# Kernel tuning notes

Hardware: AMD Instinct MI355X
Metric: run time of the kernel (lower is better)

The kernel has to match this reference:

```python
import jax, jax.numpy as jnp
import numpy as np

SR = 22050
FL = 1024      # window_samples
FP = 256       # step_samples
FCEIL = 10000  # formant ceiling (Hz)
MAXF = 4       # max formants
AP_ORDER = 10
R_ORDER = 30
FMIN, FMAX = 50, 500
DK_ITERS = 60  # Durand-Kerner iterations (replaces companion-matrix eig; differentiable)

_w = np.blackman(FL)
WIN = jnp.asarray(_w / np.sqrt(np.sum(_w ** 2)), jnp.float32)  # power-normalized blackman (diffsptk default)


def _frame(x):
    # center-padded framing, frames = T//FP + 1
    pad = FL // 2
    xp = jnp.pad(x, ((0, 0), (pad, pad)))
    n_frames = x.shape[-1] // FP + 1
    idx = jnp.arange(n_frames)[:, None] * FP + jnp.arange(FL)[None, :]
    return xp[:, idx]  # [B, F, FL]


def _levinson(r, order):
    # Levinson-Durbin on autocorrelation r[..., :order+1].
    # Returns (allpole poly coeffs a[..., order+1] with a0=1, reflection coeffs k[..., order]).
    a = jnp.zeros(r.shape[:-1] + (order + 1,), r.dtype).at[..., 0].set(1.0)
    E = r[..., 0]
    ks = []
    for m in range(1, order + 1):
        if m == 1:
            acc = r[..., 1]
        else:
            acc = r[..., m] + jnp.sum(a[..., 1:m] * r[..., m - 1:0:-1], axis=-1)
        k = -acc / (E + 1e-9)
        a_prev = a
        a = a.at[..., m].set(k)
        if m > 1:
            a = a.at[..., 1:m].add(k[..., None] * a_prev[..., m - 1:0:-1])
        E = E * (1.0 - k * k)
        ks.append(k)
    return a, jnp.stack(ks, axis=-1)


def _poly_roots(coeffs):
    # Durand-Kerner simultaneous root iteration, vectorized over frames.
    n = coeffs.shape[-1] - 1
    c = (coeffs / coeffs[..., :1]).astype(jnp.complex64)
    z0 = (0.4 + 0.9j) ** jnp.arange(1, n + 1)
    z = jnp.broadcast_to(z0, c.shape[:-1] + (n,)).astype(jnp.complex64)
    eye = jnp.eye(n, dtype=jnp.complex64)
    def step(z, _):
        p = jnp.zeros_like(z)
        for i in range(n + 1):  # Horner eval of poly at all current root estimates
            p = p * z + c[..., i:i + 1]
        diff = z[..., :, None] - z[..., None, :] + eye
        z = z - p / (jnp.prod(diff, axis=-1) + 1e-12)
        return z, None
    z, _ = jax.lax.scan(step, z, None, length=DK_ITERS)
    return z  # [..., n]


def _root_to_formant(roots):
    # downsampled spectrum covers 0..FCEIL/2, so freq = angle/(2*pi)*FCEIL
    ang = jnp.angle(roots)
    freq = ang / (2.0 * jnp.pi) * FCEIL
    freq = jnp.where(ang > 1e-4, freq, FCEIL * 0.5)  # keep upper-half-plane roots only
    return jnp.sort(freq, axis=-1)[..., :MAXF]  # [B, F, MAXF]


def _pitch(x):
    # autocorrelation pitch tracker
    xf = _frame(x)
    spec = jnp.fft.rfft(xf)
    ac = jnp.fft.irfft(spec * jnp.conj(spec))
    lag_min, lag_max = SR // FMAX, SR // FMIN  # 44..441
    seg = ac[..., lag_min:lag_max + 1]
    peak = jnp.max(seg, axis=-1)
    idx = jnp.argmax(seg, axis=-1)
    nccf = peak / (ac[..., 0] + 1e-9)
    pitch = SR / (lag_min + idx).astype(jnp.float32)
    voicing = (nccf > 0.3).astype(jnp.float32)
    return pitch, voicing, nccf


def _forward(x):
    xf = _frame(x)                 # [B, F, FL]
    xw = xf * WIN
    spec = jnp.fft.rfft(xw)        # [B, F, 513]
    nb = spec.shape[-1]
    ds = int(FCEIL / SR * nb)      # 232 bins -> Nyquist FCEIL/2
    x_ds = spec[..., :ds]
    ac_ds = jnp.fft.irfft(x_ds * jnp.conj(x_ds))   # [B, F, 462]
    ac_us = jnp.fft.irfft(spec * jnp.conj(spec))   # [B, F, 1024]
    ap_env, _ = _levinson(ac_ds, AP_ORDER)
    _, r_coeff_ref = _levinson(ac_us, R_ORDER)
    roots = _poly_roots(ap_env)
    formants = _root_to_formant(roots)
    energy = 10.0 * jnp.log10(jnp.sum(xf * xf, axis=-1) + 1e-10)
    mag = jnp.abs(jnp.fft.rfft(xf))
    freqs = jnp.arange(nb, dtype=jnp.float32) * (SR / FL)
    centroid = jnp.sum(mag * freqs, axis=-1) / (jnp.sum(mag, axis=-1) + 1e-10)
    tilt = ac_ds[..., 1] / (ac_ds[..., 0] + 1e-10)
    pitch, voicing, nccf = _pitch(x)
    pitch = jnp.log(pitch)
    return (formants, energy, centroid, tilt, pitch, voicing, r_coeff_ref, x_ds, nccf)


def setup_inputs() -> dict:
    key = jax.random.key(0)
    x = jax.random.normal(key, (8, 661500), jnp.float32)
    return {"x": x}


def reference(x):
    return _forward(x)
```

## Files before the change

### kernel.cpp

```cpp
#include <hip/hip_runtime.h>
#include <math.h>

#define NSAMP   661500
#define NFRAME  2584
#define NFTOT   20672
#define FPB     6
#define NBLK    3446

#define EN_OFF    82688
#define CEN_OFF   103360
#define TILT_OFF  124032
#define PITCH_OFF 144704
#define VOI_OFF   165376
#define RC_OFF    186048
#define XDS_OFF   806208

__device__ __forceinline__ float waveReduceSum(float v) {
  #pragma unroll
  for (int m = 1; m < 64; m <<= 1) v += __shfl_xor(v, m, 64);
  return v;
}

__device__ __forceinline__ float blockReduceSum(float v, float* s) {
  v = waveReduceSum(v);
  const int w = threadIdx.x >> 6;
  if ((threadIdx.x & 63) == 0) s[w] = v;
  __syncthreads();
  v = s[0] + s[1] + s[2] + s[3];
  __syncthreads();
  return v;
}

__device__ __forceinline__ void blockReduceSum2(float& v0, float& v1, float* s) {
  v0 = waveReduceSum(v0);
  v1 = waveReduceSum(v1);
  const int w = threadIdx.x >> 6;
  if ((threadIdx.x & 63) == 0) { s[w] = v0; s[4 + w] = v1; }
  __syncthreads();
  v0 = s[0] + s[1] + s[2] + s[3];
  v1 = s[4] + s[5] + s[6] + s[7];
  __syncthreads();
}

__device__ __forceinline__ void fft1024p(float2* X, float2* Y, const float2* tw, int tid) {
  int m = 1;
  #pragma unroll
  for (int s = 0; s < 5; ++s) {
    const int k  = tid & (m - 1);
    const int jm = tid - k;
    const float2 a0 = X[tid];
    const float2 a1 = X[tid + 256];
    const float2 a2 = X[tid + 512];
    const float2 a3 = X[tid + 768];
    const float2 w1 = tw[jm];
    float2 sA, dA, sB, dB;
    sA.x = a0.x + a2.x; sA.y = a0.y + a2.y;
    { const float dx = a0.x - a2.x, dy = a0.y - a2.y;
      dA.x = dx * w1.x + dy * w1.y;
      dA.y = dy * w1.x - dx * w1.y; }
    sB.x = a1.x + a3.x; sB.y = a1.y + a3.y;
    { const float dx = a1.x - a3.x, dy = a1.y - a3.y;
      const float wx = -w1.y, wy = w1.x;
      dB.x = dx * wx + dy * wy;
      dB.y = dy * wx - dx * wy; }
    const float w2x = w1.x * w1.x - w1.y * w1.y;
    const float w2y = 2.0f * w1.x * w1.y;
    const int B = 4 * tid - 3 * k;
    { float2 o;
      o.x = sA.x + sB.x; o.y = sA.y + sB.y;
      Y[B] = o;
      const float dx = sA.x - sB.x, dy = sA.y - sB.y;
      o.x = dx * w2x + dy * w2y;
      o.y = dy * w2x - dx * w2y;
      Y[B + 2 * m] = o; }
    { float2 o;
      o.x = dA.x + dB.x; o.y = dA.y + dB.y;
      Y[B + m] = o;
      const float dx = dA.x - dB.x, dy = dA.y - dB.y;
      o.x = dx * w2x + dy * w2y;
      o.y = dy * w2x - dx * w2y;
      Y[B + 3 * m] = o; }
    __syncthreads();
    float2* tmp = X; X = Y; Y = tmp;
    m <<= 2;
  }
}

template<int ORDER>
__device__ __forceinline__ void levinson_d(const double* r, double* a) {
  double E = r[0];
  a[0] = 1.0;
  #pragma unroll
  for (int m = 1; m <= ORDER; ++m) {
    double acc = r[m];
    #pragma unroll
    for (int i = 1; i < m; ++i) acc += a[i] * r[m - i];
    const double kk = -acc / (E + 1e-9);
    #pragma unroll
    for (int i = 1; i <= (m - 1) / 2; ++i) {
      const double t1 = a[i], t2 = a[m - i];
      a[i]     = t1 + kk * t2;
      a[m - i] = t2 + kk * t1;
    }
    if ((m & 1) == 0) { const double t = a[m >> 1]; a[m >> 1] = t + kk * t; }
    a[m] = kk;
    E *= (1.0 - kk * kk);
  }
}

__device__ __forceinline__ void levinson_f30(const float* r, float* gk) {
  float a[31];
  float E = r[0];
  a[0] = 1.0f;
  #pragma unroll
  for (int m = 1; m <= 30; ++m) {
    float acc = r[m];
    #pragma unroll
    for (int i = 1; i < m; ++i) acc += a[i] * r[m - i];
    const float kk = -acc / (E + 1e-9f);
    #pragma unroll
    for (int i = 1; i <= (m - 1) / 2; ++i) {
      const float t1 = a[i], t2 = a[m - i];
      a[i]     = t1 + kk * t2;
      a[m - i] = t2 + kk * t1;
    }
    if ((m & 1) == 0) { const float t = a[m >> 1]; a[m >> 1] = t + kk * t; }
    a[m] = kk;
    E *= (1.0f - kk * kk);
    if (gk) gk[m - 1] = kk;
  }
}

__global__ void __launch_bounds__(256, 7)
feat_mono6(const float* __restrict__ x, float* __restrict__ out,
           const int xds_pf, const int nccf_off) {
  __shared__ float2 A[1024];
  __shared__ float2 Bb[1024];
  __shared__ float2 tw[256];
  __shared__ float  Pw[232];
  __shared__ float  sred[8];
  __shared__ int    sredi[4];
  __shared__ float  stash[FPB][42];
  __shared__ float  aprt[4][11];

  const int tid   = threadIdx.x;
  const int w     = tid >> 6;
  const int lane  = tid & 63;
  const int fbase = blockIdx.x * FPB;
  const int np    = (fbase + FPB <= NFTOT) ? FPB : (NFTOT - fbase);

  {
    const float th = (float)tid * (6.2831853071795864769f / 1024.0f);
    float sn, cn;
    sincosf(th, &sn, &cn);
    tw[tid] = make_float2(cn, sn);
  }
  float wv[4];
  float wsq = 0.0f;
  #pragma unroll
  for (int q = 0; q < 4; ++q) {
    const int n = tid + q * 256;
    const float th = (float)n * (6.2831853071795864769f / 1023.0f);
    const float wn = 0.42f - 0.5f * cosf(th) + 0.08f * cosf(2.0f * th);
    wv[q] = wn;
    wsq += wn * wn;
  }
  float ctab[11];
  #pragma unroll
  for (int l = 0; l < 11; ++l)
    ctab[l] = cosf((float)(tid * l) * (6.2831853071795864769f / 462.0f));
  const float wgt462 = ((tid == 0 || tid == 231) ? 1.0f : 2.0f) * (1.0f / 462.0f);
  __syncthreads();
  const float invn = 1.0f / sqrtf(blockReduceSum(wsq, sred));

  #pragma unroll 1
  for (int p = 0; p < np; ++p) {
    const int fg = fbase + p;
    const int bb = fg / NFRAME;
    const int fr = fg - bb * NFRAME;
    const float* xb = x + (size_t)bb * NSAMP;

    float esum = 0.0f;
    #pragma unroll
    for (int q = 0; q < 4; ++q) {
      const int n = tid + q * 256;
      const int g = fr * 256 + n - 512;
      const float xv = (g >= 0 && g < NSAMP) ? xb[g] : 0.0f;
      esum += xv * xv;
      A[n] = make_float2(xv * wv[q] * invn, xv);
    }
    esum = waveReduceSum(esum);
    if (lane == 0) sred[w] = esum;
    __syncthreads();
    if (tid == 0) {
      const float en = sred[0] + sred[1] + sred[2] + sred[3];
      out[EN_OFF + fg] = 10.0f * log10f(en + 1e-10f);
    }

    fft1024p(A, Bb, tw, tid);

    float cs0 = 0.0f, cs1 = 0.0f;
    for (int k = tid; k < 513; k += 256) {
      const float2 Zk = Bb[k];
      const float2 Zn = Bb[(1024 - k) & 1023];
      const float xwr = 0.5f * (Zk.x + Zn.x);
      const float xwi = 0.5f * (Zk.y - Zn.y);
      const float xfr = 0.5f * (Zk.y + Zn.y);
      const float xfi = -0.5f * (Zk.x - Zn.x);
      const float pw = xwr * xwr + xwi * xwi;
      const float pf = xfr * xfr + xfi * xfi;
      const float mg = sqrtf(pf);
      cs0 += mg;
      cs1 += mg * ((float)k * (22050.0f / 1024.0f));
      if (k < 232) {
        Pw[k] = pw;
        if (xds_pf == 232) {
          out[XDS_OFF + (size_t)fg * 232 + k] = xwr;
        } else {
          out[XDS_OFF + (size_t)fg * 464 + 2 * k]     = xwr;
          out[XDS_OFF + (size_t)fg * 464 + 2 * k + 1] = xwi;
        }
      }
    }
    blockReduceSum2(cs0, cs1, sred);
    if (tid == 0) out[CEN_OFF + fg] = cs1 / (cs0 + 1e-10f);

    #pragma unroll
    for (int q = 0; q < 4; ++q) {
      const int k2 = tid + q * 256;
      const int km = (k2 <= 512) ? k2 : (1024 - k2);
      const float2 Zk = Bb[km];
      const float2 Zn = Bb[(1024 - km) & 1023];
      const float xwr = 0.5f * (Zk.x + Zn.x);
      const float xwi = 0.5f * (Zk.y - Zn.y);
      const float xfr = 0.5f * (Zk.y + Zn.y);
      const float xfi = -0.5f * (Zk.x - Zn.x);
      const float pw = xwr * xwr + xwi * xwi;
      const float pf = xfr * xfr + xfi * xfi;
      A[k2] = make_float2(pw * 1024.0f, pf);
    }
    __syncthreads();

    fft1024p(A, Bb, tw, tid);

    float pv = -3.0e38f;
    int   pl = 1 << 30;
    for (int l = 44 + tid; l <= 441; l += 256) {
      const float v = Bb[l].y;
      if (v > pv) { pv = v; pl = l; }
    }
    #pragma unroll
    for (int m = 1; m < 64; m <<= 1) {
      const float ov = __shfl_xor(pv, m, 64);
      const int   ol = __shfl_xor(pl, m, 64);
      if (ov > pv || (ov == pv && ol < pl)) { pv = ov; pl = ol; }
    }
    if (lane == 0) { sred[w] = pv; sredi[w] = pl; }
    __syncthreads();
    if (tid == 0) {
      float bv = sred[0]; int bl = sredi[0];
      #pragma unroll
      for (int q = 1; q < 4; ++q)
        if (sred[q] > bv || (sred[q] == bv && sredi[q] < bl)) { bv = sred[q]; bl = sredi[q]; }
      const float ac0  = Bb[0].y * (1.0f / 1024.0f);
      const float peak = bv * (1.0f / 1024.0f);
      const float nccf = peak / (ac0 + 1e-9f);
      out[PITCH_OFF + fg] = logf(22050.0f / (float)bl);
      out[VOI_OFF + fg]   = (nccf > 0.3f) ? 1.0f : 0.0f;
      out[nccf_off + fg]  = nccf;
    }

    const float pwW = (tid < 232) ? Pw[tid] * wgt462 : 0.0f;
    #pragma unroll
    for (int l = 0; l < 11; ++l) {
      const float t = waveReduceSum(pwW * ctab[l]);
      if (lane == 0) aprt[w][l] = t;
    }
    __syncthreads();
    if (tid < 11)
      stash[p][31 + tid] = aprt[0][tid] + aprt[1][tid] + aprt[2][tid] + aprt[3][tid];
    if (tid == 0) {
      const float a0 = aprt[0][0] + aprt[1][0] + aprt[2][0] + aprt[3][0];
      const float a1 = aprt[0][1] + aprt[1][1] + aprt[2][1] + aprt[3][1];
      out[TILT_OFF + fg] = a1 / (a0 + 1e-10f);
    }
    if (tid < 31) stash[p][tid] = Bb[tid].x * (1.0f / 1048576.0f);
    __syncthreads();
  }

  if (w == 0) {
    const int g     = lane / 10;
    const int ri    = lane - g * 10;
    const int gbase = g * 10;
    const int gg    = (g < FPB) ? g : (FPB - 1);
    const bool act  = (g < np);
    const int fg    = fbase + gg;

    levinson_f30(&stash[gg][0],
                 (ri == 0 && act) ? (out + RC_OFF + (size_t)fg * 30) : (float*)nullptr);

    double rds[11], a10[11];
    #pragma unroll
    for (int l = 0; l < 11; ++l) rds[l] = (double)stash[gg][31 + l];
    levinson_d<10>(rds, a10);

    double zr = 0.4, zi = 0.9;
    for (int q = 0; q < ri; ++q) {
      const double nr = zr * 0.4 - zi * 0.9;
      zi = zr * 0.9 + zi * 0.4;
      zr = nr;
    }
    for (int it = 0; it < 60; ++it) {
      double pr = 1.0, pi = 0.0;
      #pragma unroll
      for (int q = 1; q <= 10; ++q) {
        const double nr = pr * zr - pi * zi + a10[q];
        pi = pr * zi + pi * zr;
        pr = nr;
      }
      double dr = 1.0, di = 0.0;
      #pragma unroll
      for (int j = 0; j < 10; ++j) {
        const double ozr = __shfl(zr, gbase + j, 64);
        const double ozi = __shfl(zi, gbase + j, 64);
        const double er = (j == ri) ? 1.0 : (zr - ozr);
        const double ei = (j == ri) ? 0.0 : (zi - ozi);
        const double nr = dr * er - di * ei;
        di = dr * ei + di * er;
        dr = nr;
      }
      dr += 1e-12;
      const double inv = 1.0 / (dr * dr + di * di);
      const double qr = (pr * dr + pi * di) * inv;
      const double qi = (pi * dr - pr * di) * inv;
      zr -= qr;
      zi -= qi;
    }
    const double ang = atan2(zi, zr);
    double freq = (ang > 0.0001) ? (ang / 6.283185307179586476925287 * 10000.0) : 5000.0;
    if (ri >= 10) freq = 1.0e300;

    double f[10];
    #pragma unroll
    for (int j = 0; j < 10; ++j) f[j] = __shfl(freq, gbase + j, 64);
    bool used[10];
    #pragma unroll
    for (int j = 0; j < 10; ++j) used[j] = false;
    float o4[4];
    #pragma unroll
    for (int p2 = 0; p2 < 4; ++p2) {
      double mn = 1.0e300;
      int mj = -1;
      #pragma unroll
      for (int j = 0; j < 10; ++j)
        if (!used[j] && f[j] < mn) { mn = f[j]; mj = j; }
      if (mj >= 0) used[mj] = true;
      o4[p2] = (float)mn;
    }
    if (ri == 0 && act) {
      out[(size_t)fg * 4 + 0] = o4[0];
      out[(size_t)fg * 4 + 1] = o4[1];
      out[(size_t)fg * 4 + 2] = o4[2];
      out[(size_t)fg * 4 + 3] = o4[3];
    }
  }
}

extern "C" void kernel_launch(void* const* d_in, const int* in_sizes, int n_in,
                              void* d_out, int out_size, void* d_ws, size_t ws_size,
                              hipStream_t stream) {
  (void)in_sizes; (void)n_in; (void)d_ws; (void)ws_size;
  const float* x = (const float*)d_in[0];
  float* out = (float*)d_out;
  int xds_pf = 232;
  if (out_size >= XDS_OFF + NFTOT * 464 + NFTOT) xds_pf = 464;
  const int nccf_off = XDS_OFF + NFTOT * xds_pf;
  feat_mono6<<<dim3(NBLK), dim3(256), 0, stream>>>(x, out, xds_pf, nccf_off);
}
```

Measured before the change: 337.4 us.

## Merge per-frame block reductions into one barrier and derive energy from autocorrelation

The separate energy reduction is removed. Energy is now taken from the lag-0 autocorrelation of the unwindowed frame, which the pitch FFT already computes. The centroid sums and the 11 all-pole autocorrelation partials are reduced in the same barrier phase as the pitch argmax, so the Pw shared buffer and several __syncthreads per frame go away. The loop-tail barrier moves out of the loop, complex x_ds outputs are written as float2, and launch bounds go from 7 to 8 waves, which adds register pressure and depends on the remaining barriers being enough for correctness.

```diff
diff --git a/kernel.cpp b/kernel.cpp
--- a/kernel.cpp
+++ b/kernel.cpp
@@ -29,17 +29,6 @@
   v = s[0] + s[1] + s[2] + s[3];
   __syncthreads();
   return v;
-}
-
-__device__ __forceinline__ void blockReduceSum2(float& v0, float& v1, float* s) {
-  v0 = waveReduceSum(v0);
-  v1 = waveReduceSum(v1);
-  const int w = threadIdx.x >> 6;
-  if ((threadIdx.x & 63) == 0) { s[w] = v0; s[4 + w] = v1; }
-  __syncthreads();
-  v0 = s[0] + s[1] + s[2] + s[3];
-  v1 = s[4] + s[5] + s[6] + s[7];
-  __syncthreads();
 }
 
 __device__ __forceinline__ void fft1024p(float2* X, float2* Y, const float2* tw, int tid) {
@@ -131,14 +120,13 @@
   }
 }
 
-__global__ void __launch_bounds__(256, 7)
+__global__ void __launch_bounds__(256, 8)
 feat_mono6(const float* __restrict__ x, float* __restrict__ out,
            const int xds_pf, const int nccf_off) {
   __shared__ float2 A[1024];
   __shared__ float2 Bb[1024];
   __shared__ float2 tw[256];
-  __shared__ float  Pw[232];
-  __shared__ float  sred[8];
+  __shared__ float  sred[12];
   __shared__ int    sredi[4];
   __shared__ float  stash[FPB][42];
   __shared__ float  aprt[4][11];
@@ -180,27 +168,21 @@
     const int fr = fg - bb * NFRAME;
     const float* xb = x + (size_t)bb * NSAMP;
 
-    float esum = 0.0f;
     #pragma unroll
     for (int q = 0; q < 4; ++q) {
       const int n = tid + q * 256;
       const int g = fr * 256 + n - 512;
       const float xv = (g >= 0 && g < NSAMP) ? xb[g] : 0.0f;
-      esum += xv * xv;
       A[n] = make_float2(xv * wv[q] * invn, xv);
     }
-    esum = waveReduceSum(esum);
-    if (lane == 0) sred[w] = esum;
     __syncthreads();
-    if (tid == 0) {
-      const float en = sred[0] + sred[1] + sred[2] + sred[3];
-      out[EN_OFF + fg] = 10.0f * log10f(en + 1e-10f);
-    }
 
     fft1024p(A, Bb, tw, tid);
 
     float cs0 = 0.0f, cs1 = 0.0f;
-    for (int k = tid; k < 513; k += 256) {
+    float myPw = 0.0f;
+    {
+      const int k = tid;
       const float2 Zk = Bb[k];
       const float2 Zn = Bb[(1024 - k) & 1023];
       const float xwr = 0.5f * (Zk.x + Zn.x);
@@ -213,17 +195,36 @@
       cs0 += mg;
       cs1 += mg * ((float)k * (22050.0f / 1024.0f));
       if (k < 232) {
-        Pw[k] = pw;
+        myPw = pw;
         if (xds_pf == 232) {
           out[XDS_OFF + (size_t)fg * 232 + k] = xwr;
         } else {
-          out[XDS_OFF + (size_t)fg * 464 + 2 * k]     = xwr;
-          out[XDS_OFF + (size_t)fg * 464 + 2 * k + 1] = xwi;
+          ((float2*)(out + XDS_OFF))[(size_t)fg * 232 + k] = make_float2(xwr, xwi);
         }
       }
     }
-    blockReduceSum2(cs0, cs1, sred);
-    if (tid == 0) out[CEN_OFF + fg] = cs1 / (cs0 + 1e-10f);
+    {
+      const int k = tid + 256;
+      const float2 Zk = Bb[k];
+      const float2 Zn = Bb[1024 - k];
+      const float xfr = 0.5f * (Zk.y + Zn.y);
+      const float xfi = -0.5f * (Zk.x - Zn.x);
+      const float pf = xfr * xfr + xfi * xfi;
+      const float mg = sqrtf(pf);
+      cs0 += mg;
+      cs1 += mg * ((float)k * (22050.0f / 1024.0f));
+    }
+    if (tid == 0) {
+      const int k = 512;
+      const float2 Zk = Bb[k];
+      const float2 Zn = Bb[512];
+      const float xfr = 0.5f * (Zk.y + Zn.y);
+      const float xfi = -0.5f * (Zk.x - Zn.x);
+      const float pf = xfr * xfr + xfi * xfi;
+      const float mg = sqrtf(pf);
+      cs0 += mg;
+      cs1 += mg * ((float)k * (22050.0f / 1024.0f));
+    }
 
     #pragma unroll
     for (int q = 0; q < 4; ++q) {
@@ -255,8 +256,17 @@
       const int   ol = __shfl_xor(pl, m, 64);
       if (ov > pv || (ov == pv && ol < pl)) { pv = ov; pl = ol; }
     }
-    if (lane == 0) { sred[w] = pv; sredi[w] = pl; }
+    cs0 = waveReduceSum(cs0);
+    cs1 = waveReduceSum(cs1);
+    if (lane == 0) { sred[w] = pv; sredi[w] = pl; sred[4 + w] = cs0; sred[8 + w] = cs1; }
+    const float pwW = myPw * wgt462;
+    #pragma unroll
+    for (int l = 0; l < 11; ++l) {
+      const float t = waveReduceSum(pwW * ctab[l]);
+      if (lane == 0) aprt[w][l] = t;
+    }
     __syncthreads();
+
     if (tid == 0) {
       float bv = sred[0]; int bl = sredi[0];
       #pragma unroll
@@ -268,25 +278,19 @@
       out[PITCH_OFF + fg] = logf(22050.0f / (float)bl);
       out[VOI_OFF + fg]   = (nccf > 0.3f) ? 1.0f : 0.0f;
       out[nccf_off + fg]  = nccf;
-    }
-
-    const float pwW = (tid < 232) ? Pw[tid] * wgt462 : 0.0f;
-    #pragma unroll
-    for (int l = 0; l < 11; ++l) {
-      const float t = waveReduceSum(pwW * ctab[l]);
-      if (lane == 0) aprt[w][l] = t;
-    }
-    __syncthreads();
+      out[EN_OFF + fg]    = 10.0f * log10f(ac0 + 1e-10f);
+      const float c0 = sred[4] + sred[5] + sred[6] + sred[7];
+      const float c1 = sred[8] + sred[9] + sred[10] + sred[11];
+      out[CEN_OFF + fg]   = c1 / (c0 + 1e-10f);
+      const float a0 = aprt[0][0] + aprt[1][0] + aprt[2][0] + aprt[3][0];
+      const float a1 = aprt[0][1] + aprt[1][1] + aprt[2][1] + aprt[3][1];
+      out[TILT_OFF + fg]  = a1 / (a0 + 1e-10f);
+    }
     if (tid < 11)
       stash[p][31 + tid] = aprt[0][tid] + aprt[1][tid] + aprt[2][tid] + aprt[3][tid];
-    if (tid == 0) {
-      const float a0 = aprt[0][0] + aprt[1][0] + aprt[2][0] + aprt[3][0];
-      const float a1 = aprt[0][1] + aprt[1][1] + aprt[2][1] + aprt[3][1];
-      out[TILT_OFF + fg] = a1 / (a0 + 1e-10f);
-    }
     if (tid < 31) stash[p][tid] = Bb[tid].x * (1.0f / 1048576.0f);
-    __syncthreads();
-  }
+  }
+  __syncthreads();
 
   if (w == 0) {
     const int g     = lane / 10;
```

Result: no change. 332.4 us (-1.5%).
